# Performance work log

Hardware: AMD Instinct MI355X
Metric: run time of the kernel (lower is better)

Reference implementation:

```python
import jax, jax.numpy as jnp
import numpy as np

N_FACTORS = 4
N_ITERATIONS = 2
N_LAYERS = 2
N_USERS = 50000
N_ITEMS = 50000
EMB_DIM = 128
N_EDGES = 2_000_000
EPS = 1e-12


def setup_inputs() -> dict:
    key = jax.random.key(0)
    k1, k2, k3, k4 = jax.random.split(key, 4)
    n_nodes = N_USERS + N_ITEMS
    return {
        "user_emb": jax.random.normal(k1, (N_USERS, EMB_DIM), dtype=jnp.float32) * 0.1,
        "item_emb": jax.random.normal(k2, (N_ITEMS, EMB_DIM), dtype=jnp.float32) * 0.1,
        "all_h_list": jax.random.randint(k3, (N_EDGES,), 0, n_nodes, dtype=jnp.int32),
        "all_t_list": jax.random.randint(k4, (N_EDGES,), 0, n_nodes, dtype=jnp.int32),
    }


def _l2norm(x):
    # F.normalize(x, dim=1): x / max(||x||_2, eps)
    n = jnp.sqrt(jnp.sum(x * x, axis=1, keepdims=True))
    return x / jnp.maximum(n, EPS)


def _star_routing(user_emb, item_emb, h, t):
    n_nodes = user_emb.shape[0] + item_emb.shape[0]
    E = h.shape[0]
    ego = jnp.concatenate([user_emb, item_emb], axis=0)          # [N, D]
    A_values = jnp.ones((N_FACTORS, E), dtype=ego.dtype)
    all_embeddings = [ego]
    for _layer in range(N_LAYERS):
        ego_chunks = jnp.split(ego, N_FACTORS, axis=1)           # F x [N, D/F]
        layer_chunks = [None] * N_FACTORS
        for it in range(N_ITERATIONS):
            scores = jax.nn.softmax(A_values, axis=0)            # per-edge softmax over factors
            new_vals = []
            for i in range(N_FACTORS):
                v = scores[i]                                    # [E]
                deg = jax.ops.segment_sum(v, h, num_segments=n_nodes)  # row sums of A_i
                d_inv = 1.0 / jnp.sqrt(jnp.maximum(deg, EPS))    # D^{-1/2}
                x = ego_chunks[i] * d_inv[:, None]               # D_col @ e
                # A_i @ x : gather tails, weight by edge value, scatter-add to heads
                x = jax.ops.segment_sum(v[:, None] * x[t], h, num_segments=n_nodes)
                x = x * d_inv[:, None]                           # D_col @ (A @ (D_col @ e))
                layer_chunks[i] = x
                # routing logit update
                head = _l2norm(x[h])                             # [E, D/F]
                tail = _l2norm(ego_chunks[i][t])
                new_vals.append(jnp.sum(head * jnp.tanh(tail), axis=1))
            A_values = A_values + jnp.stack(new_vals, axis=0)
        ego = jnp.concatenate(layer_chunks, axis=1)
        all_embeddings.append(ego)
    # mean over [ego_0, ego_1, ..., ego_L]
    out = jnp.mean(jnp.stack(all_embeddings, axis=1), axis=1)    # [N, D]
    return out


def reference(user_emb, item_emb, all_h_list, all_t_list):
    all_emb = _star_routing(user_emb, item_emb, all_h_list, all_t_list)
    u_g = all_emb[:N_USERS]
    i_g = all_emb[N_USERS:]
    # with pick=False the '_t' (test) path is identical to the train path
    return u_g, i_g, u_g, i_g
```

## Files before the change

kernel.cpp:

```cpp
#include <hip/hip_runtime.h>
#include <cmath>

#define GS_LOOP(i, n) for (int i = blockIdx.x * blockDim.x + threadIdx.x; i < (n); i += gridDim.x * blockDim.x)

constexpr int NUSERS = 50000;
constexpr int NNODES = 100000;
constexpr int EMBD   = 128;
constexpr int NEDGE  = 2000000;

__device__ __forceinline__ float bf2f(unsigned short u) {
  union { unsigned int i; float f; } v; v.i = ((unsigned int)u) << 16; return v.f;
}
__device__ __forceinline__ unsigned short f2bf(float x) {
  union { float f; unsigned int i; } v; v.f = x;
  unsigned int r = v.i + 0x7FFFu + ((v.i >> 16) & 1u);
  return (unsigned short)(r >> 16);
}

__global__ void init_k(const float* __restrict__ ue, const float* __restrict__ ie,
                       float* __restrict__ ego0, float* __restrict__ A) {
  const int NU4 = NUSERS * EMBD / 4;
  const int NT4 = NNODES * EMBD / 4;
  const float4* u4 = (const float4*)ue;
  const float4* i4 = (const float4*)ie;
  float4* e4 = (float4*)ego0;
  GS_LOOP(i, NT4) e4[i] = (i < NU4) ? u4[i] : i4[i - NU4];
  float4* A4 = (float4*)A;
  const float4 ones = make_float4(1.f, 1.f, 1.f, 1.f);
  GS_LOOP(i, NEDGE) A4[i] = ones;
}

__global__ void hist_k(const int* __restrict__ h, int* __restrict__ counts) {
  GS_LOOP(e, NEDGE) atomicAdd(&counts[h[e]], 1);
}

__global__ __launch_bounds__(1024) void scan_k(const int* __restrict__ counts,
                                               int* __restrict__ row_ptr) {
  __shared__ int wsum[16];
  __shared__ int carry_s;
  const int tid = threadIdx.x;
  const int lane = tid & 63;
  const int wid = tid >> 6;
  if (tid == 0) { carry_s = 0; row_ptr[0] = 0; }
  __syncthreads();
  for (int base = 0; base < NNODES; base += 1024) {
    int i = base + tid;
    int v = (i < NNODES) ? counts[i] : 0;
    #pragma unroll
    for (int off = 1; off < 64; off <<= 1) {
      int y = __shfl_up(v, off, 64);
      if (lane >= off) v += y;
    }
    if (lane == 63) wsum[wid] = v;
    __syncthreads();
    if (wid == 0) {
      int w = (lane < 16) ? wsum[lane] : 0;
      #pragma unroll
      for (int off = 1; off < 16; off <<= 1) {
        int y = __shfl_up(w, off, 64);
        if (lane >= off) w += y;
      }
      if (lane < 16) wsum[lane] = w;
    }
    __syncthreads();
    int carry = carry_s;
    int incl = v + carry + (wid ? wsum[wid - 1] : 0);
    if (i < NNODES) row_ptr[i + 1] = incl;
    __syncthreads();
    if (tid == 1023) carry_s = incl;
    __syncthreads();
  }
}

__global__ void fill_k(const int* __restrict__ h, const int* __restrict__ t,
                       const int* __restrict__ row_ptr, int* __restrict__ cur,
                       int* __restrict__ csr_t) {
  GS_LOOP(e, NEDGE) {
    int u = h[e];
    int pos = row_ptr[u] + atomicAdd(&cur[u], 1);
    csr_t[pos] = t[e];
  }
}

__global__ __launch_bounds__(256) void deg_sm_k(const float* __restrict__ A,
                                                const int* __restrict__ row_ptr,
                                                float* __restrict__ c,
                                                float* __restrict__ dv) {
  const float4* A4 = (const float4*)A;
  float4* c4 = (float4*)c;
  const int g = threadIdx.x >> 4;
  const int lane16 = threadIdx.x & 15;
  const int u = blockIdx.x * 16 + g;
  if (u >= NNODES) return;
  const int beg = row_ptr[u], end = row_ptr[u + 1];
  float4 acc = make_float4(0.f, 0.f, 0.f, 0.f);
  for (int p = beg + lane16; p < end; p += 16) {
    float4 a = A4[p];
    float m = fmaxf(fmaxf(a.x, a.y), fmaxf(a.z, a.w));
    float e0 = __expf(a.x - m), e1 = __expf(a.y - m);
    float e2 = __expf(a.z - m), e3 = __expf(a.w - m);
    float inv = 1.f / (e0 + e1 + e2 + e3);
    float4 s = make_float4(e0 * inv, e1 * inv, e2 * inv, e3 * inv);
    c4[p] = s;
    acc.x += s.x; acc.y += s.y; acc.z += s.z; acc.w += s.w;
  }
  #pragma unroll
  for (int m = 1; m < 16; m <<= 1) {
    acc.x += __shfl_xor(acc.x, m, 64);
    acc.y += __shfl_xor(acc.y, m, 64);
    acc.z += __shfl_xor(acc.z, m, 64);
    acc.w += __shfl_xor(acc.w, m, 64);
  }
  if (lane16 == 0)
    ((float4*)dv)[u] = make_float4(rsqrtf(fmaxf(acc.x, 1e-12f)),
                                   rsqrtf(fmaxf(acc.y, 1e-12f)),
                                   rsqrtf(fmaxf(acc.z, 1e-12f)),
                                   rsqrtf(fmaxf(acc.w, 1e-12f)));
}

__global__ void conv_k(const float4* __restrict__ src, ushort4* __restrict__ dst) {
  GS_LOOP(i, NNODES * 32) {
    float4 a = src[i];
    dst[i] = make_ushort4(f2bf(a.x), f2bf(a.y), f2bf(a.z), f2bf(a.w));
  }
}

__global__ __launch_bounds__(256) void tanh_k(const float4* __restrict__ P4,
                                              ushort4* __restrict__ Tnb4) {
  const int j = threadIdx.x & 31;
  const int r0 = blockIdx.x * 8 + (threadIdx.x >> 5);
  for (int u = r0; u < NNODES; u += gridDim.x * 8) {
    float4 y = P4[(size_t)u * 32 + j];
    float ss = y.x * y.x + y.y * y.y + y.z * y.z + y.w * y.w;
    ss += __shfl_xor(ss, 1, 64);
    ss += __shfl_xor(ss, 2, 64);
    ss += __shfl_xor(ss, 4, 64);
    float inv = 1.f / fmaxf(sqrtf(ss), 1e-12f);
    Tnb4[(size_t)u * 32 + j] = make_ushort4(f2bf(tanhf(y.x * inv)), f2bf(tanhf(y.y * inv)),
                                            f2bf(tanhf(y.z * inv)), f2bf(tanhf(y.w * inv)));
  }
}

__global__ __launch_bounds__(256) void prop_k(
    const ushort4* __restrict__ Pb4, float4* __restrict__ Q4,
    const float* __restrict__ dv, const int* __restrict__ row_ptr,
    const int* __restrict__ csr_t, const float* __restrict__ c,
    float* __restrict__ A, const ushort4* __restrict__ Tnb4,
    const float4* __restrict__ e0_4, const float4* __restrict__ e1_4,
    float4* __restrict__ o1_4, int mode) {
  const int u = blockIdx.x * 4 + (threadIdx.x >> 6);
  const int l = threadIdx.x & 63;
  const int half = l >> 5;
  const int j = l & 31;
  const int f = j >> 3;
  const int beg = row_ptr[u], end = row_ptr[u + 1];

  float4 acc = make_float4(0.f, 0.f, 0.f, 0.f);
  int p = beg + half;
  for (; p + 6 < end; p += 8) {
    const int t0 = csr_t[p],     t1 = csr_t[p + 2];
    const int t2 = csr_t[p + 4], t3 = csr_t[p + 6];
    const float c0 = c[(size_t)p * 4 + f]       * dv[t0 * 4 + f];
    const float c1 = c[(size_t)(p + 2) * 4 + f] * dv[t1 * 4 + f];
    const float c2 = c[(size_t)(p + 4) * 4 + f] * dv[t2 * 4 + f];
    const float c3 = c[(size_t)(p + 6) * 4 + f] * dv[t3 * 4 + f];
    const ushort4 y0 = Pb4[(size_t)t0 * 32 + j];
    const ushort4 y1 = Pb4[(size_t)t1 * 32 + j];
    const ushort4 y2 = Pb4[(size_t)t2 * 32 + j];
    const ushort4 y3 = Pb4[(size_t)t3 * 32 + j];
    acc.x += c0 * bf2f(y0.x) + c1 * bf2f(y1.x) + c2 * bf2f(y2.x) + c3 * bf2f(y3.x);
    acc.y += c0 * bf2f(y0.y) + c1 * bf2f(y1.y) + c2 * bf2f(y2.y) + c3 * bf2f(y3.y);
    acc.z += c0 * bf2f(y0.z) + c1 * bf2f(y1.z) + c2 * bf2f(y2.z) + c3 * bf2f(y3.z);
    acc.w += c0 * bf2f(y0.w) + c1 * bf2f(y1.w) + c2 * bf2f(y2.w) + c3 * bf2f(y3.w);
  }
  for (; p < end; p += 2) {
    const int tn = csr_t[p];
    const float cf = c[(size_t)p * 4 + f] * dv[tn * 4 + f];
    const ushort4 y = Pb4[(size_t)tn * 32 + j];
    acc.x += cf * bf2f(y.x); acc.y += cf * bf2f(y.y);
    acc.z += cf * bf2f(y.z); acc.w += cf * bf2f(y.w);
  }
  acc.x += __shfl_xor(acc.x, 32, 64);
  acc.y += __shfl_xor(acc.y, 32, 64);
  acc.z += __shfl_xor(acc.z, 32, 64);
  acc.w += __shfl_xor(acc.w, 32, 64);
  const float du = dv[u * 4 + f];
  const float4 x = make_float4(acc.x * du, acc.y * du, acc.z * du, acc.w * du);

  if (mode == 2) {
    if (half == 0) {
      const float4 a = e0_4[(size_t)u * 32 + j];
      const float4 b = e1_4[(size_t)u * 32 + j];
      o1_4[(size_t)u * 32 + j] = make_float4((a.x + b.x + x.x) * (1.f / 3.f),
                                             (a.y + b.y + x.y) * (1.f / 3.f),
                                             (a.z + b.z + x.z) * (1.f / 3.f),
                                             (a.w + b.w + x.w) * (1.f / 3.f));
    }
    return;
  }
  if (mode == 1 && half == 0) Q4[(size_t)u * 32 + j] = x;

  float ss = x.x * x.x + x.y * x.y + x.z * x.z + x.w * x.w;
  ss += __shfl_xor(ss, 1, 64);
  ss += __shfl_xor(ss, 2, 64);
  ss += __shfl_xor(ss, 4, 64);
  const float inv = 1.f / fmaxf(sqrtf(ss), 1e-12f);
  const float4 xn = make_float4(x.x * inv, x.y * inv, x.z * inv, x.w * inv);

  int q = beg + half;
  for (; q + 2 < end; q += 4) {
    const int t0 = csr_t[q], t1 = csr_t[q + 2];
    const ushort4 b0 = Tnb4[(size_t)t0 * 32 + j];
    const ushort4 b1 = Tnb4[(size_t)t1 * 32 + j];
    float s0 = xn.x * bf2f(b0.x) + xn.y * bf2f(b0.y) + xn.z * bf2f(b0.z) + xn.w * bf2f(b0.w);
    float s1 = xn.x * bf2f(b1.x) + xn.y * bf2f(b1.y) + xn.z * bf2f(b1.z) + xn.w * bf2f(b1.w);
    s0 += __shfl_xor(s0, 1, 64); s1 += __shfl_xor(s1, 1, 64);
    s0 += __shfl_xor(s0, 2, 64); s1 += __shfl_xor(s1, 2, 64);
    s0 += __shfl_xor(s0, 4, 64); s1 += __shfl_xor(s1, 4, 64);
    if ((j & 7) == 0) {
      A[(size_t)q * 4 + f] += s0;
      A[(size_t)(q + 2) * 4 + f] += s1;
    }
  }
  for (; q < end; q += 2) {
    const int tn = csr_t[q];
    const ushort4 tb = Tnb4[(size_t)tn * 32 + j];
    float s = xn.x * bf2f(tb.x) + xn.y * bf2f(tb.y) + xn.z * bf2f(tb.z) + xn.w * bf2f(tb.w);
    s += __shfl_xor(s, 1, 64);
    s += __shfl_xor(s, 2, 64);
    s += __shfl_xor(s, 4, 64);
    if ((j & 7) == 0) A[(size_t)q * 4 + f] += s;
  }
}

extern "C" void kernel_launch(void* const* d_in, const int* in_sizes, int n_in,
                              void* d_out, int out_size, void* d_ws, size_t ws_size,
                              hipStream_t stream) {
  const float* ue = (const float*)d_in[0];
  const float* ie = (const float*)d_in[1];
  const int* h = (const int*)d_in[2];
  const int* t = (const int*)d_in[3];
  float* out = (float*)d_out;
  char* ws = (char*)d_ws;

  size_t off = 0;
  auto alloc = [&](size_t bytes) -> void* {
    void* p = ws + off;
    off += (bytes + 255) & ~size_t(255);
    return p;
  };
  float* ego0  = (float*)alloc(sizeof(float) * (size_t)NNODES * EMBD);
  float* ego1  = (float*)alloc(sizeof(float) * (size_t)NNODES * EMBD);
  float* A     = (float*)alloc(sizeof(float) * 4 * (size_t)NEDGE);
  float* c     = (float*)alloc(sizeof(float) * 4 * (size_t)NEDGE);
  float* dv    = (float*)alloc(sizeof(float) * NNODES * 4);
  int* row_ptr = (int*)alloc(sizeof(int) * (NNODES + 1));
  int* cur     = (int*)alloc(sizeof(int) * NNODES);
  int* csr_t   = (int*)alloc(sizeof(int) * NEDGE);

  float* o1 = out;
  float* o2 = out + (size_t)NNODES * EMBD;
  ushort4* Pb0  = (ushort4*)o1;
  ushort4* Tnb0 = (ushort4*)((char*)o1 + sizeof(unsigned short) * (size_t)NNODES * EMBD);
  ushort4* Pb1  = (ushort4*)o2;
  ushort4* Tnb1 = (ushort4*)((char*)o2 + sizeof(unsigned short) * (size_t)NNODES * EMBD);

  init_k<<<2048, 256, 0, stream>>>(ue, ie, ego0, A);
  hipMemsetAsync(cur, 0, sizeof(int) * NNODES, stream);
  hist_k<<<2048, 256, 0, stream>>>(h, cur);
  scan_k<<<1, 1024, 0, stream>>>(cur, row_ptr);
  hipMemsetAsync(cur, 0, sizeof(int) * NNODES, stream);
  fill_k<<<2048, 256, 0, stream>>>(h, t, row_ptr, cur, csr_t);

  conv_k<<<2048, 256, 0, stream>>>((const float4*)ego0, Pb0);
  tanh_k<<<12500, 256, 0, stream>>>((const float4*)ego0, Tnb0);

  for (int pass = 0; pass < 4; ++pass) {
    const ushort4* Pb  = (pass < 2) ? Pb0 : Pb1;
    const ushort4* Tnb = (pass < 2) ? Tnb0 : Tnb1;
    const int mode = (pass == 1) ? 1 : (pass == 3) ? 2 : 0;
    deg_sm_k<<<(NNODES + 15) / 16, 256, 0, stream>>>(A, row_ptr, c, dv);
    prop_k<<<NNODES / 4, 256, 0, stream>>>(Pb, (float4*)ego1, dv, row_ptr, csr_t, c, A,
                                           Tnb, (const float4*)ego0, (const float4*)ego1,
                                           (float4*)o1, mode);
    if (pass == 1) {
      conv_k<<<2048, 256, 0, stream>>>((const float4*)ego1, Pb1);
      tanh_k<<<12500, 256, 0, stream>>>((const float4*)ego1, Tnb1);
    }
  }

  hipMemcpyAsync(o2, o1, sizeof(float) * (size_t)NNODES * EMBD,
                 hipMemcpyDeviceToDevice, stream);
}
```

Measured before the change: 1.248 ms.

## Fuse bf16/tanh conversions into init and prop, parallelize scan, deepen unrolls

The concat, bf16 conversion and normalized-tanh precompute are merged into one init kernel. The pass-1 prop kernel now writes the bf16 and tanh copies of the new embeddings directly, which removes two extra kernels and a re-read of ego1. The A initialization moves into the histogram kernel. The single-block serial scan is replaced by a three-kernel multi-block scan. The gather loops are unrolled deeper (8 edges for propagation, 4 for routing) to keep more loads in flight, at the cost of higher register pressure.

```diff
diff --git a/kernel.cpp b/kernel.cpp
--- a/kernel.cpp
+++ b/kernel.cpp
@@ -7,6 +7,7 @@
 constexpr int NNODES = 100000;
 constexpr int EMBD   = 128;
 constexpr int NEDGE  = 2000000;
+constexpr int NSCAN  = (NNODES + 1023) / 1024;
 
 __device__ __forceinline__ float bf2f(unsigned short u) {
   union { unsigned int i; float f; } v; v.i = ((unsigned int)u) << 16; return v.f;
@@ -17,59 +18,85 @@
   return (unsigned short)(r >> 16);
 }
 
-__global__ void init_k(const float* __restrict__ ue, const float* __restrict__ ie,
-                       float* __restrict__ ego0, float* __restrict__ A) {
-  const int NU4 = NUSERS * EMBD / 4;
-  const int NT4 = NNODES * EMBD / 4;
-  const float4* u4 = (const float4*)ue;
-  const float4* i4 = (const float4*)ie;
-  float4* e4 = (float4*)ego0;
-  GS_LOOP(i, NT4) e4[i] = (i < NU4) ? u4[i] : i4[i - NU4];
+__global__ __launch_bounds__(256) void init_k(const float4* __restrict__ ue4,
+                                              const float4* __restrict__ ie4,
+                                              float4* __restrict__ ego0,
+                                              ushort4* __restrict__ Pb0,
+                                              ushort4* __restrict__ Tnb0) {
+  const int j = threadIdx.x & 31;
+  const int u = blockIdx.x * 8 + (threadIdx.x >> 5);
+  if (u >= NNODES) return;
+  const float4 y = (u < NUSERS) ? ue4[(size_t)u * 32 + j]
+                                : ie4[(size_t)(u - NUSERS) * 32 + j];
+  ego0[(size_t)u * 32 + j] = y;
+  Pb0[(size_t)u * 32 + j] = make_ushort4(f2bf(y.x), f2bf(y.y), f2bf(y.z), f2bf(y.w));
+  float ss = y.x * y.x + y.y * y.y + y.z * y.z + y.w * y.w;
+  ss += __shfl_xor(ss, 1, 64);
+  ss += __shfl_xor(ss, 2, 64);
+  ss += __shfl_xor(ss, 4, 64);
+  const float inv = 1.f / fmaxf(sqrtf(ss), 1e-12f);
+  Tnb0[(size_t)u * 32 + j] = make_ushort4(f2bf(tanhf(y.x * inv)), f2bf(tanhf(y.y * inv)),
+                                          f2bf(tanhf(y.z * inv)), f2bf(tanhf(y.w * inv)));
+}
+
+__global__ void hist_k(const int* __restrict__ h, int* __restrict__ counts,
+                       float* __restrict__ A) {
   float4* A4 = (float4*)A;
   const float4 ones = make_float4(1.f, 1.f, 1.f, 1.f);
-  GS_LOOP(i, NEDGE) A4[i] = ones;
-}
-
-__global__ void hist_k(const int* __restrict__ h, int* __restrict__ counts) {
-  GS_LOOP(e, NEDGE) atomicAdd(&counts[h[e]], 1);
-}
-
-__global__ __launch_bounds__(1024) void scan_k(const int* __restrict__ counts,
-                                               int* __restrict__ row_ptr) {
+  GS_LOOP(e, NEDGE) { atomicAdd(&counts[h[e]], 1); A4[e] = ones; }
+}
+
+__global__ __launch_bounds__(1024) void scan1_k(const int* __restrict__ counts,
+                                                int* __restrict__ part,
+                                                int* __restrict__ bsum) {
   __shared__ int wsum[16];
-  __shared__ int carry_s;
+  const int tid = threadIdx.x, lane = tid & 63, wid = tid >> 6;
+  const int i = blockIdx.x * 1024 + tid;
+  int v = (i < NNODES) ? counts[i] : 0;
+  #pragma unroll
+  for (int off = 1; off < 64; off <<= 1) {
+    int y = __shfl_up(v, off, 64);
+    if (lane >= off) v += y;
+  }
+  if (lane == 63) wsum[wid] = v;
+  __syncthreads();
+  if (wid == 0) {
+    int w = (lane < 16) ? wsum[lane] : 0;
+    #pragma unroll
+    for (int off = 1; off < 16; off <<= 1) {
+      int y = __shfl_up(w, off, 64);
+      if (lane >= off) w += y;
+    }
+    if (lane < 16) wsum[lane] = w;
+  }
+  __syncthreads();
+  const int incl = v + (wid ? wsum[wid - 1] : 0);
+  if (i < NNODES) part[i] = incl;
+  if (tid == 1023) bsum[blockIdx.x] = incl;
+}
+
+__global__ __launch_bounds__(128) void scan2_k(const int* __restrict__ bsum,
+                                               int* __restrict__ boff) {
+  __shared__ int s0[128], s1[128];
   const int tid = threadIdx.x;
-  const int lane = tid & 63;
-  const int wid = tid >> 6;
-  if (tid == 0) { carry_s = 0; row_ptr[0] = 0; }
+  s0[tid] = (tid < NSCAN) ? bsum[tid] : 0;
   __syncthreads();
-  for (int base = 0; base < NNODES; base += 1024) {
-    int i = base + tid;
-    int v = (i < NNODES) ? counts[i] : 0;
-    #pragma unroll
-    for (int off = 1; off < 64; off <<= 1) {
-      int y = __shfl_up(v, off, 64);
-      if (lane >= off) v += y;
-    }
-    if (lane == 63) wsum[wid] = v;
+  int* a = s0; int* b = s1;
+  for (int off = 1; off < 128; off <<= 1) {
+    const int val = a[tid] + ((tid >= off) ? a[tid - off] : 0);
+    b[tid] = val;
     __syncthreads();
-    if (wid == 0) {
-      int w = (lane < 16) ? wsum[lane] : 0;
-      #pragma unroll
-      for (int off = 1; off < 16; off <<= 1) {
-        int y = __shfl_up(w, off, 64);
-        if (lane >= off) w += y;
-      }
-      if (lane < 16) wsum[lane] = w;
-    }
-    __syncthreads();
-    int carry = carry_s;
-    int incl = v + carry + (wid ? wsum[wid - 1] : 0);
-    if (i < NNODES) row_ptr[i + 1] = incl;
-    __syncthreads();
-    if (tid == 1023) carry_s = incl;
-    __syncthreads();
-  }
+    int* tmp = a; a = b; b = tmp;
+  }
+  boff[tid] = (tid == 0) ? 0 : a[tid - 1];
+}
+
+__global__ __launch_bounds__(1024) void scan3_k(const int* __restrict__ part,
+                                                const int* __restrict__ boff,
+                                                int* __restrict__ row_ptr) {
+  const int i = blockIdx.x * 1024 + threadIdx.x;
+  if (i < NNODES) row_ptr[i + 1] = part[i] + boff[blockIdx.x];
+  if (i == 0) row_ptr[0] = 0;
 }
 
 __global__ void fill_k(const int* __restrict__ h, const int* __restrict__ t,
@@ -118,36 +145,14 @@
                                    rsqrtf(fmaxf(acc.w, 1e-12f)));
 }
 
-__global__ void conv_k(const float4* __restrict__ src, ushort4* __restrict__ dst) {
-  GS_LOOP(i, NNODES * 32) {
-    float4 a = src[i];
-    dst[i] = make_ushort4(f2bf(a.x), f2bf(a.y), f2bf(a.z), f2bf(a.w));
-  }
-}
-
-__global__ __launch_bounds__(256) void tanh_k(const float4* __restrict__ P4,
-                                              ushort4* __restrict__ Tnb4) {
-  const int j = threadIdx.x & 31;
-  const int r0 = blockIdx.x * 8 + (threadIdx.x >> 5);
-  for (int u = r0; u < NNODES; u += gridDim.x * 8) {
-    float4 y = P4[(size_t)u * 32 + j];
-    float ss = y.x * y.x + y.y * y.y + y.z * y.z + y.w * y.w;
-    ss += __shfl_xor(ss, 1, 64);
-    ss += __shfl_xor(ss, 2, 64);
-    ss += __shfl_xor(ss, 4, 64);
-    float inv = 1.f / fmaxf(sqrtf(ss), 1e-12f);
-    Tnb4[(size_t)u * 32 + j] = make_ushort4(f2bf(tanhf(y.x * inv)), f2bf(tanhf(y.y * inv)),
-                                            f2bf(tanhf(y.z * inv)), f2bf(tanhf(y.w * inv)));
-  }
-}
-
 __global__ __launch_bounds__(256) void prop_k(
     const ushort4* __restrict__ Pb4, float4* __restrict__ Q4,
     const float* __restrict__ dv, const int* __restrict__ row_ptr,
     const int* __restrict__ csr_t, const float* __restrict__ c,
     float* __restrict__ A, const ushort4* __restrict__ Tnb4,
     const float4* __restrict__ e0_4, const float4* __restrict__ e1_4,
-    float4* __restrict__ o1_4, int mode) {
+    float4* __restrict__ o1_4, ushort4* __restrict__ Pb1w,
+    ushort4* __restrict__ Tnb1w, int mode) {
   const int u = blockIdx.x * 4 + (threadIdx.x >> 6);
   const int l = threadIdx.x & 63;
   const int half = l >> 5;
@@ -157,21 +162,35 @@
 
   float4 acc = make_float4(0.f, 0.f, 0.f, 0.f);
   int p = beg + half;
-  for (; p + 6 < end; p += 8) {
-    const int t0 = csr_t[p],     t1 = csr_t[p + 2];
-    const int t2 = csr_t[p + 4], t3 = csr_t[p + 6];
-    const float c0 = c[(size_t)p * 4 + f]       * dv[t0 * 4 + f];
-    const float c1 = c[(size_t)(p + 2) * 4 + f] * dv[t1 * 4 + f];
-    const float c2 = c[(size_t)(p + 4) * 4 + f] * dv[t2 * 4 + f];
-    const float c3 = c[(size_t)(p + 6) * 4 + f] * dv[t3 * 4 + f];
+  for (; p + 14 < end; p += 16) {
+    const int t0 = csr_t[p],      t1 = csr_t[p + 2];
+    const int t2 = csr_t[p + 4],  t3 = csr_t[p + 6];
+    const int t4 = csr_t[p + 8],  t5 = csr_t[p + 10];
+    const int t6 = csr_t[p + 12], t7 = csr_t[p + 14];
     const ushort4 y0 = Pb4[(size_t)t0 * 32 + j];
     const ushort4 y1 = Pb4[(size_t)t1 * 32 + j];
     const ushort4 y2 = Pb4[(size_t)t2 * 32 + j];
     const ushort4 y3 = Pb4[(size_t)t3 * 32 + j];
-    acc.x += c0 * bf2f(y0.x) + c1 * bf2f(y1.x) + c2 * bf2f(y2.x) + c3 * bf2f(y3.x);
-    acc.y += c0 * bf2f(y0.y) + c1 * bf2f(y1.y) + c2 * bf2f(y2.y) + c3 * bf2f(y3.y);
-    acc.z += c0 * bf2f(y0.z) + c1 * bf2f(y1.z) + c2 * bf2f(y2.z) + c3 * bf2f(y3.z);
-    acc.w += c0 * bf2f(y0.w) + c1 * bf2f(y1.w) + c2 * bf2f(y2.w) + c3 * bf2f(y3.w);
+    const ushort4 y4 = Pb4[(size_t)t4 * 32 + j];
+    const ushort4 y5 = Pb4[(size_t)t5 * 32 + j];
+    const ushort4 y6 = Pb4[(size_t)t6 * 32 + j];
+    const ushort4 y7 = Pb4[(size_t)t7 * 32 + j];
+    const float c0 = c[(size_t)p * 4 + f]        * dv[t0 * 4 + f];
+    const float c1 = c[(size_t)(p + 2) * 4 + f]  * dv[t1 * 4 + f];
+    const float c2 = c[(size_t)(p + 4) * 4 + f]  * dv[t2 * 4 + f];
+    const float c3 = c[(size_t)(p + 6) * 4 + f]  * dv[t3 * 4 + f];
+    const float c4_ = c[(size_t)(p + 8) * 4 + f] * dv[t4 * 4 + f];
+    const float c5 = c[(size_t)(p + 10) * 4 + f] * dv[t5 * 4 + f];
+    const float c6 = c[(size_t)(p + 12) * 4 + f] * dv[t6 * 4 + f];
+    const float c7 = c[(size_t)(p + 14) * 4 + f] * dv[t7 * 4 + f];
+    acc.x += c0 * bf2f(y0.x) + c1 * bf2f(y1.x) + c2 * bf2f(y2.x) + c3 * bf2f(y3.x)
+           + c4_ * bf2f(y4.x) + c5 * bf2f(y5.x) + c6 * bf2f(y6.x) + c7 * bf2f(y7.x);
+    acc.y += c0 * bf2f(y0.y) + c1 * bf2f(y1.y) + c2 * bf2f(y2.y) + c3 * bf2f(y3.y)
+           + c4_ * bf2f(y4.y) + c5 * bf2f(y5.y) + c6 * bf2f(y6.y) + c7 * bf2f(y7.y);
+    acc.z += c0 * bf2f(y0.z) + c1 * bf2f(y1.z) + c2 * bf2f(y2.z) + c3 * bf2f(y3.z)
+           + c4_ * bf2f(y4.z) + c5 * bf2f(y5.z) + c6 * bf2f(y6.z) + c7 * bf2f(y7.z);
+    acc.w += c0 * bf2f(y0.w) + c1 * bf2f(y1.w) + c2 * bf2f(y2.w) + c3 * bf2f(y3.w)
+           + c4_ * bf2f(y4.w) + c5 * bf2f(y5.w) + c6 * bf2f(y6.w) + c7 * bf2f(y7.w);
   }
   for (; p < end; p += 2) {
     const int tn = csr_t[p];
@@ -198,7 +217,10 @@
     }
     return;
   }
-  if (mode == 1 && half == 0) Q4[(size_t)u * 32 + j] = x;
+  if (mode == 1 && half == 0) {
+    Q4[(size_t)u * 32 + j] = x;
+    Pb1w[(size_t)u * 32 + j] = make_ushort4(f2bf(x.x), f2bf(x.y), f2bf(x.z), f2bf(x.w));
+  }
 
   float ss = x.x * x.x + x.y * x.y + x.z * x.z + x.w * x.w;
   ss += __shfl_xor(ss, 1, 64);
@@ -206,20 +228,32 @@
   ss += __shfl_xor(ss, 4, 64);
   const float inv = 1.f / fmaxf(sqrtf(ss), 1e-12f);
   const float4 xn = make_float4(x.x * inv, x.y * inv, x.z * inv, x.w * inv);
+  if (mode == 1 && half == 0)
+    Tnb1w[(size_t)u * 32 + j] = make_ushort4(f2bf(tanhf(xn.x)), f2bf(tanhf(xn.y)),
+                                             f2bf(tanhf(xn.z)), f2bf(tanhf(xn.w)));
 
   int q = beg + half;
-  for (; q + 2 < end; q += 4) {
-    const int t0 = csr_t[q], t1 = csr_t[q + 2];
+  for (; q + 6 < end; q += 8) {
+    const int t0 = csr_t[q],     t1 = csr_t[q + 2];
+    const int t2 = csr_t[q + 4], t3 = csr_t[q + 6];
     const ushort4 b0 = Tnb4[(size_t)t0 * 32 + j];
     const ushort4 b1 = Tnb4[(size_t)t1 * 32 + j];
+    const ushort4 b2 = Tnb4[(size_t)t2 * 32 + j];
+    const ushort4 b3 = Tnb4[(size_t)t3 * 32 + j];
     float s0 = xn.x * bf2f(b0.x) + xn.y * bf2f(b0.y) + xn.z * bf2f(b0.z) + xn.w * bf2f(b0.w);
     float s1 = xn.x * bf2f(b1.x) + xn.y * bf2f(b1.y) + xn.z * bf2f(b1.z) + xn.w * bf2f(b1.w);
-    s0 += __shfl_xor(s0, 1, 64); s1 += __shfl_xor(s1, 1, 64);
-    s0 += __shfl_xor(s0, 2, 64); s1 += __shfl_xor(s1, 2, 64);
-    s0 += __shfl_xor(s0, 4, 64); s1 += __shfl_xor(s1, 4, 64);
+    float s2 = xn.x * bf2f(b2.x) + xn.y * bf2f(b2.y) + xn.z * bf2f(b2.z) + xn.w * bf2f(b2.w);
+    float s3 = xn.x * bf2f(b3.x) + xn.y * bf2f(b3.y) + xn.z * bf2f(b3.z) + xn.w * bf2f(b3.w);
+    #pragma unroll
+    for (int m = 1; m < 8; m <<= 1) {
+      s0 += __shfl_xor(s0, m, 64); s1 += __shfl_xor(s1, m, 64);
+      s2 += __shfl_xor(s2, m, 64); s3 += __shfl_xor(s3, m, 64);
+    }
     if ((j & 7) == 0) {
       A[(size_t)q * 4 + f] += s0;
       A[(size_t)(q + 2) * 4 + f] += s1;
+      A[(size_t)(q + 4) * 4 + f] += s2;
+      A[(size_t)(q + 6) * 4 + f] += s3;
     }
   }
   for (; q < end; q += 2) {
@@ -256,6 +290,9 @@
   float* dv    = (float*)alloc(sizeof(float) * NNODES * 4);
   int* row_ptr = (int*)alloc(sizeof(int) * (NNODES + 1));
   int* cur     = (int*)alloc(sizeof(int) * NNODES);
+  int* part    = (int*)alloc(sizeof(int) * NNODES);
+  int* bsum    = (int*)alloc(sizeof(int) * 128);
+  int* boff    = (int*)alloc(sizeof(int) * 128);
   int* csr_t   = (int*)alloc(sizeof(int) * NEDGE);
 
   float* o1 = out;
@@ -265,15 +302,15 @@
   ushort4* Pb1  = (ushort4*)o2;
   ushort4* Tnb1 = (ushort4*)((char*)o2 + sizeof(unsigned short) * (size_t)NNODES * EMBD);
 
-  init_k<<<2048, 256, 0, stream>>>(ue, ie, ego0, A);
+  init_k<<<(NNODES + 7) / 8, 256, 0, stream>>>((const float4*)ue, (const float4*)ie,
+                                               (float4*)ego0, Pb0, Tnb0);
   hipMemsetAsync(cur, 0, sizeof(int) * NNODES, stream);
-  hist_k<<<2048, 256, 0, stream>>>(h, cur);
-  scan_k<<<1, 1024, 0, stream>>>(cur, row_ptr);
+  hist_k<<<2048, 256, 0, stream>>>(h, cur, A);
+  scan1_k<<<NSCAN, 1024, 0, stream>>>(cur, part, bsum);
+  scan2_k<<<1, 128, 0, stream>>>(bsum, boff);
+  scan3_k<<<NSCAN, 1024, 0, stream>>>(part, boff, row_ptr);
   hipMemsetAsync(cur, 0, sizeof(int) * NNODES, stream);
   fill_k<<<2048, 256, 0, stream>>>(h, t, row_ptr, cur, csr_t);
-
-  conv_k<<<2048, 256, 0, stream>>>((const float4*)ego0, Pb0);
-  tanh_k<<<12500, 256, 0, stream>>>((const float4*)ego0, Tnb0);
 
   for (int pass = 0; pass < 4; ++pass) {
     const ushort4* Pb  = (pass < 2) ? Pb0 : Pb1;
@@ -282,11 +319,7 @@
     deg_sm_k<<<(NNODES + 15) / 16, 256, 0, stream>>>(A, row_ptr, c, dv);
     prop_k<<<NNODES / 4, 256, 0, stream>>>(Pb, (float4*)ego1, dv, row_ptr, csr_t, c, A,
                                            Tnb, (const float4*)ego0, (const float4*)ego1,
-                                           (float4*)o1, mode);
-    if (pass == 1) {
-      conv_k<<<2048, 256, 0, stream>>>((const float4*)ego1, Pb1);
-      tanh_k<<<12500, 256, 0, stream>>>((const float4*)ego1, Tnb1);
-    }
+                                           (float4*)o1, Pb1, Tnb1, mode);
   }
 
   hipMemcpyAsync(o2, o1, sizeof(float) * (size_t)NNODES * EMBD,
```

Result: faster. 1.209 ms (-3.1%).
